# Performance work log

Hardware: AMD Instinct MI355X
Metric: run time of the kernel (lower is better)

The kernel has to match this reference:

```python
import jax, jax.numpy as jnp
import numpy as np

EMBED = 128
HEADS = 16
N = 10000
E = 160000
NEG_SLOPE = 0.2


def setup_inputs() -> dict:
    key = jax.random.key(0)
    ks = jax.random.split(key, 12)
    s = 0.05
    return {
        "x": jax.random.normal(ks[0], (N, EMBED), jnp.float32),
        "edge_index": jax.random.randint(ks[1], (2, E), 0, N, jnp.int64),
        # gat1: in=EMBED, out=EMBED, heads=16, concat
        "W1": jax.random.normal(ks[2], (EMBED, HEADS * EMBED), jnp.float32) * s,
        "a_src1": jax.random.normal(ks[3], (HEADS, EMBED), jnp.float32) * s,
        "a_dst1": jax.random.normal(ks[4], (HEADS, EMBED), jnp.float32) * s,
        "b1": jnp.zeros((HEADS * EMBED,), jnp.float32),
        # gat2: in=HEADS*EMBED, out=EMBED, heads=1, no concat
        "W2": jax.random.normal(ks[5], (HEADS * EMBED, EMBED), jnp.float32) * s,
        "a_src2": jax.random.normal(ks[6], (1, EMBED), jnp.float32) * s,
        "a_dst2": jax.random.normal(ks[7], (1, EMBED), jnp.float32) * s,
        "b2": jnp.zeros((EMBED,), jnp.float32),
        # classifier
        "Wc": jax.random.normal(ks[8], (EMBED, 1), jnp.float32) * s,
        "bc": jnp.zeros((1,), jnp.float32),
    }


def _gat_layer(x, src, dst, W, a_src, a_dst, b, heads, out_ch, n_nodes):
    # node projection: [N, H, C]
    h = (x @ W).reshape(n_nodes, heads, out_ch)
    # per-node attention logits [N, H]
    al_s = jnp.einsum('nhc,hc->nh', h, a_src)
    al_d = jnp.einsum('nhc,hc->nh', h, a_dst)
    # per-edge logits [E, H]
    e = jax.nn.leaky_relu(al_s[src] + al_d[dst], NEG_SLOPE)
    # segment softmax over incoming edges of each dst node
    m = jax.ops.segment_max(e, dst, num_segments=n_nodes)
    ex = jnp.exp(e - m[dst])
    z = jax.ops.segment_sum(ex, dst, num_segments=n_nodes)
    alpha = ex / (z[dst] + 1e-16)
    # weighted scatter-aggregate [N, H, C]
    msg = h[src] * alpha[:, :, None]
    out = jax.ops.segment_sum(msg, dst, num_segments=n_nodes)
    return out.reshape(n_nodes, heads * out_ch) + b


def reference(x, edge_index, W1, a_src1, a_dst1, b1, W2, a_src2, a_dst2, b2, Wc, bc):
    n_nodes = x.shape[0]
    # PyG GATConv default: add self loops
    loop = jnp.arange(n_nodes, dtype=edge_index.dtype)
    src = jnp.concatenate([edge_index[0], loop])
    dst = jnp.concatenate([edge_index[1], loop])
    h = _gat_layer(x, src, dst, W1, a_src1, a_dst1, b1, HEADS, EMBED, n_nodes)
    h = jax.nn.elu(h)
    h = _gat_layer(h, src, dst, W2, a_src2, a_dst2, b2, 1, EMBED, n_nodes)
    return h @ Wc + bc  # [N, 1]
```

## Files before the change

### kernel.cpp

```cpp
#include <hip/hip_runtime.h>
#include <hip/hip_bf16.h>

#define EMBED 128
#define HEADS 16
#define NEG 0.2f
#define MAXE 256

typedef __attribute__((ext_vector_type(8))) short short8;
typedef __attribute__((ext_vector_type(4))) float floatx4;

static __device__ __forceinline__ float leaky(float x) { return x > 0.f ? x : NEG * x; }

static __device__ __forceinline__ short f2bf_bits(float f) {
  __hip_bfloat16 h = __float2bfloat16(f);
  union { __hip_bfloat16 b; short s; } u;
  u.b = h;
  return u.s;
}


__global__ void k_hist(const int* __restrict__ ei, int E, int N, int* __restrict__ deg) {
  int i = blockIdx.x * blockDim.x + threadIdx.x;
  int Et = E + N;
  if (i >= Et) return;
  int d = (i < E) ? ei[E + i] : (i - E);
  atomicAdd(&deg[d], 1);
}

__global__ __launch_bounds__(256) void k_scan1(const int* __restrict__ deg,
                                               int* __restrict__ excl,
                                               int* __restrict__ bsum, int n) {
  __shared__ int s[256];
  int i = blockIdx.x * 256 + threadIdx.x;
  int v = (i < n) ? deg[i] : 0;
  s[threadIdx.x] = v;
  __syncthreads();
  for (int d = 1; d < 256; d <<= 1) {
    int add = ((int)threadIdx.x >= d) ? s[threadIdx.x - d] : 0;
    __syncthreads();
    s[threadIdx.x] += add;
    __syncthreads();
  }
  if (i < n) excl[i] = s[threadIdx.x] - v;
  if (threadIdx.x == 255) bsum[blockIdx.x] = s[255];
}

__global__ void k_scan2(int* __restrict__ bsum, int nb) {
  if (threadIdx.x == 0 && blockIdx.x == 0) {
    int acc = 0;
    for (int i = 0; i < nb; ++i) { int v = bsum[i]; bsum[i] = acc; acc += v; }
  }
}

__global__ __launch_bounds__(256) void k_scan3(const int* __restrict__ deg,
                                               const int* __restrict__ excl,
                                               const int* __restrict__ bsum,
                                               int* __restrict__ row_ptr,
                                               int* __restrict__ cursor, int n) {
  int i = blockIdx.x * 256 + threadIdx.x;
  if (i < n) {
    int r = excl[i] + bsum[blockIdx.x];
    row_ptr[i] = r;
    cursor[i] = r;
    if (i == n - 1) row_ptr[n] = r + deg[i];
  }
}

__global__ void k_scatter(const int* __restrict__ ei, int E, int N,
                          int* __restrict__ cursor, int* __restrict__ csr_src) {
  int i = blockIdx.x * blockDim.x + threadIdx.x;
  int Et = E + N;
  if (i >= Et) return;
  int s = (i < E) ? ei[i] : (i - E);
  int d = (i < E) ? ei[E + i] : (i - E);
  int pos = atomicAdd(&cursor[d], 1);
  csr_src[pos] = s;
}


__global__ __launch_bounds__(256) void k_prepAll(const float* __restrict__ W1,
                                                 const float* __restrict__ a_src1,
                                                 const float* __restrict__ a_dst1,
                                                 const float* __restrict__ W2,
                                                 const float* __restrict__ a_src2,
                                                 const float* __restrict__ a_dst2,
                                                 const float* __restrict__ Wc,
                                                 const float* __restrict__ b2,
                                                 const float* __restrict__ bc,
                                                 float* __restrict__ wsAll,
                                                 float* __restrict__ uvec,
                                                 float* __restrict__ cconst) {
  int gid = blockIdx.x * 256 + threadIdx.x;
  if (gid < 4096) {
    int sel = gid >> 11;
    int id = gid & 2047;
    int h = id >> 7, k = id & 127;
    const float* av = sel ? a_dst1 : a_src1;
    float sum = 0.f;
    const float* wrow = W1 + (size_t)k * 2048 + h * 128;
    const float* arow = av + h * 128;
#pragma unroll 4
    for (int c = 0; c < 128; ++c) sum += wrow[c] * arow[c];
    wsAll[gid] = sum;
  } else if (gid < 10240) {
    int g = gid - 4096;
    int sel = g >> 11;
    int k = g & 2047;
    const float* v = sel == 0 ? Wc : (sel == 1 ? a_src2 : a_dst2);
    const float* wrow = W2 + (size_t)k * 128;
    float s = 0.f;
#pragma unroll 4
    for (int j = 0; j < 128; ++j) s += wrow[j] * v[j];
    uvec[g] = s;
  } else if (gid == 10240) {
    float s = 0.f;
    for (int j = 0; j < 128; ++j) s += b2[j] * Wc[j];
    *cconst = s + bc[0];
  }
}


__global__ __launch_bounds__(256) void k_prep2aT(const float* __restrict__ W1,
                                                 short* __restrict__ hi,
                                                 short* __restrict__ lo) {
  __shared__ float tile[64][65];
  int h = blockIdx.x;
  int c0 = blockIdx.y * 64;
  int j0 = blockIdx.z * 64;
  int t = threadIdx.x;
#pragma unroll
  for (int i = 0; i < 4; ++i) {
    int idx4 = i * 256 + t;
    int c = idx4 >> 4, j4 = idx4 & 15;
    float4 v = *(const float4*)&W1[(size_t)(c0 + c) * 2048 + h * 128 + j0 + j4 * 4];
    tile[c][j4 * 4 + 0] = v.x;
    tile[c][j4 * 4 + 1] = v.y;
    tile[c][j4 * 4 + 2] = v.z;
    tile[c][j4 * 4 + 3] = v.w;
  }
  __syncthreads();
#pragma unroll
  for (int i = 0; i < 4; ++i) {
    int idx = i * 256 + t;
    int j = idx >> 4, c4 = idx & 15;
    unsigned short vh[4], vl[4];
#pragma unroll
    for (int ii = 0; ii < 4; ++ii) {
      float wv = tile[c4 * 4 + ii][j];
      short hb = f2bf_bits(wv);
      float hf = __uint_as_float(((unsigned int)(unsigned short)hb) << 16);
      vh[ii] = (unsigned short)hb;
      vl[ii] = (unsigned short)f2bf_bits(wv - hf);
    }
    size_t o = (size_t)h * 16384 + (size_t)(j0 + j) * 128 + c0 + c4 * 4;
    *(ushort4*)&hi[o] = make_ushort4(vh[0], vh[1], vh[2], vh[3]);
    *(ushort4*)&lo[o] = make_ushort4(vl[0], vl[1], vl[2], vl[3]);
  }
}


__global__ __launch_bounds__(256) void k_al1v2(const float* __restrict__ x,
                                               const float* __restrict__ wsAll,
                                               float* __restrict__ als,
                                               float* __restrict__ ald, int N) {
  __shared__ float wss[128][16], wsd[128][16];
  int tid = threadIdx.x;
  for (int i = tid; i < 2048; i += 256) {
    int h = i >> 7, c = i & 127;
    wss[c][h] = wsAll[i];
    wsd[c][h] = wsAll[2048 + i];
  }
  __syncthreads();
  int gid = blockIdx.x * 256 + tid;
  int n = gid >> 4, h = gid & 15;
  if (n >= N) return;
  const float4* xp = (const float4*)(x + (size_t)n * 128);
  float ps = 0.f, pd = 0.f;
#pragma unroll 8
  for (int c4 = 0; c4 < 32; ++c4) {
    float4 xv = xp[c4];
    int c = c4 * 4;
    ps += xv.x * wss[c][h] + xv.y * wss[c + 1][h] + xv.z * wss[c + 2][h] + xv.w * wss[c + 3][h];
    pd += xv.x * wsd[c][h] + xv.y * wsd[c + 1][h] + xv.z * wsd[c + 2][h] + xv.w * wsd[c + 3][h];
  }
  als[gid] = ps;
  ald[gid] = pd;
}


__global__ __launch_bounds__(256) void k_attn1d(const float* __restrict__ x,
                                                const float* __restrict__ als,
                                                const float* __restrict__ ald,
                                                const int* __restrict__ row_ptr,
                                                const int* __restrict__ csr,
                                                __hip_bfloat16* __restrict__ xaggb,
                                                int N) {
  int d = blockIdx.x;
  int tid = threadIdx.x;
  int e0 = row_ptr[d];
  int deg = row_ptr[d + 1] - e0;

  __shared__ int srcb[MAXE];
  __shared__ float ex[MAXE][17];
  __shared__ float xs[16][132];
  __shared__ float red[16][17];
  __shared__ float ald_sh[16], iz_sh[16];

  if (tid < 16) ald_sh[tid] = ald[(size_t)d * 16 + tid];
  __syncthreads();

  int hh = tid & 15, er = tid >> 4;
  float aldh = ald_sh[hh];
  int cg = tid & 15, h2 = tid >> 4;
  float acc[8] = {0.f, 0.f, 0.f, 0.f, 0.f, 0.f, 0.f, 0.f};

  if (deg <= MAXE) {
    for (int e = tid; e < deg; e += 256) srcb[e] = csr[e0 + e];
    __syncthreads();
    float zp = 0.f;
    for (int e = er; e < deg; e += 16) {
      float v = __expf(leaky(als[(size_t)srcb[e] * 16 + hh] + aldh));
      ex[e][hh] = v;
      zp += v;
    }
    red[er][hh] = zp;
    __syncthreads();
    if (tid < 16) {
      float z = 0.f;
#pragma unroll
      for (int k = 0; k < 16; ++k) z += red[k][tid];
      iz_sh[tid] = 1.f / (z + 1e-16f);
    }
    for (int base = 0; base < deg; base += 16) {
      int nb = min(16, deg - base);
      if (er < nb) {
        const float* xr = x + (size_t)srcb[base + er] * 128;
        *(float4*)&xs[er][cg * 4]      = *(const float4*)&xr[cg * 4];
        *(float4*)&xs[er][64 + cg * 4] = *(const float4*)&xr[64 + cg * 4];
      }
      __syncthreads();
      for (int e = 0; e < nb; ++e) {
        float a = ex[base + e][h2];
        float4 v0 = *(const float4*)&xs[e][cg * 4];
        float4 v1 = *(const float4*)&xs[e][64 + cg * 4];
        acc[0] += a * v0.x; acc[1] += a * v0.y; acc[2] += a * v0.z; acc[3] += a * v0.w;
        acc[4] += a * v1.x; acc[5] += a * v1.y; acc[6] += a * v1.z; acc[7] += a * v1.w;
      }
      __syncthreads();
    }
  } else {
    float zp = 0.f;
    for (int e = er; e < deg; e += 16) {
      int s = csr[e0 + e];
      zp += __expf(leaky(als[(size_t)s * 16 + hh] + aldh));
    }
    red[er][hh] = zp;
    __syncthreads();
    if (tid < 16) {
      float z = 0.f;
#pragma unroll
      for (int k = 0; k < 16; ++k) z += red[k][tid];
      iz_sh[tid] = 1.f / (z + 1e-16f);
    }
    for (int base = 0; base < deg; base += 16) {
      int nb = min(16, deg - base);
      __syncthreads();
      if (tid < nb) srcb[tid] = csr[e0 + base + tid];
      __syncthreads();
      if (tid < nb * 16) {
        int e = tid >> 4;
        ex[e][hh] = __expf(leaky(als[(size_t)srcb[e] * 16 + hh] + aldh));
      }
      if (er < nb) {
        const float* xr = x + (size_t)srcb[er] * 128;
        *(float4*)&xs[er][cg * 4]      = *(const float4*)&xr[cg * 4];
        *(float4*)&xs[er][64 + cg * 4] = *(const float4*)&xr[64 + cg * 4];
      }
      __syncthreads();
      for (int e = 0; e < nb; ++e) {
        float a = ex[e][h2];
        float4 v0 = *(const float4*)&xs[e][cg * 4];
        float4 v1 = *(const float4*)&xs[e][64 + cg * 4];
        acc[0] += a * v0.x; acc[1] += a * v0.y; acc[2] += a * v0.z; acc[3] += a * v0.w;
        acc[4] += a * v1.x; acc[5] += a * v1.y; acc[6] += a * v1.z; acc[7] += a * v1.w;
      }
    }
    __syncthreads();
  }

  float izh = iz_sh[h2];
  __hip_bfloat16 t0[4], t1[4];
#pragma unroll
  for (int i = 0; i < 4; ++i) {
    t0[i] = __float2bfloat16(acc[i] * izh);
    t1[i] = __float2bfloat16(acc[4 + i] * izh);
  }
  __hip_bfloat16* op = xaggb + (size_t)h2 * N * 128 + (size_t)d * 128;
  *(uint2*)&op[cg * 4]      = *(uint2*)t0;
  *(uint2*)&op[64 + cg * 4] = *(uint2*)t1;
}


__global__ __launch_bounds__(256, 2) void k_fused(const __hip_bfloat16* __restrict__ xaggb,
                                                  const short* __restrict__ w1t_hi,
                                                  const short* __restrict__ w1t_lo,
                                                  const float* __restrict__ b1,
                                                  const float* __restrict__ uvec,
                                                  float* __restrict__ partc,
                                                  float* __restrict__ parts,
                                                  float* __restrict__ partd,
                                                  int N) {
  __shared__ float sh[512];
  __shared__ __align__(16) char Bh[32768];
  __shared__ __align__(16) char Bl[32768];
  int tid = threadIdx.x;
  int h = blockIdx.y;
  int n0 = blockIdx.x * 256;

  for (int i = tid; i < 512; i += 256) {
    int arr = i >> 7, jj = i & 127;
    sh[i] = (arr == 0) ? b1[h * 128 + jj] : uvec[(arr - 1) * 2048 + h * 128 + jj];
  }
  const char* gbh = (const char*)(w1t_hi + (size_t)h * 16384);
  const char* gbl = (const char*)(w1t_lo + (size_t)h * 16384);
#pragma unroll
  for (int i = 0; i < 8; ++i) {
    int ci = i * 256 + tid;
    int row = ci >> 4, kc = ci & 15;
    int po = row * 256 + ((kc ^ (row & 15)) << 4);
    *(uint4*)(Bh + po) = *(const uint4*)(gbh + ci * 16);
    *(uint4*)(Bl + po) = *(const uint4*)(gbl + ci * 16);
  }

  int w = tid >> 6, lane = tid & 63;
  int quad = lane >> 4, l15 = lane & 15;
  int nw = n0 + w * 64;

  const char* abase = (const char*)xaggb + (size_t)h * N * 256;
  short8 a[4][4];
#pragma unroll
  for (int mt = 0; mt < 4; ++mt) {
    int node = nw + mt * 16 + l15;
    if (node >= N) node = N - 1;
    const char* rowp = abase + (size_t)node * 256 + quad * 16;
#pragma unroll
    for (int ks = 0; ks < 4; ++ks)
      a[mt][ks] = *(const short8*)(rowp + ks * 64);
  }
  __syncthreads();

  float ucr[8], usr[8], udr[8];
  floatx4 acc[4][8];
#pragma unroll
  for (int jt = 0; jt < 8; ++jt) {
    int jl = jt * 16 + l15;
    float b = sh[jl];
    ucr[jt] = sh[128 + jl];
    usr[jt] = sh[256 + jl];
    udr[jt] = sh[384 + jl];
#pragma unroll
    for (int mt = 0; mt < 4; ++mt) acc[mt][jt] = (floatx4)(b);
  }

  for (int ks = 0; ks < 4; ++ks) {
    int xo = (((ks * 4 + quad) ^ l15) << 4);
#pragma unroll
    for (int jt = 0; jt < 8; ++jt) {
      int po = (jt * 16 + l15) * 256 + xo;
      short8 wh = *(const short8*)(Bh + po);
      short8 wl = *(const short8*)(Bl + po);
#pragma unroll
      for (int mt = 0; mt < 4; ++mt) {
        acc[mt][jt] = __builtin_amdgcn_mfma_f32_16x16x32_bf16(a[mt][ks], wh, acc[mt][jt], 0, 0, 0);
        acc[mt][jt] = __builtin_amdgcn_mfma_f32_16x16x32_bf16(a[mt][ks], wl, acc[mt][jt], 0, 0, 0);
      }
    }
  }

#pragma unroll
  for (int mt = 0; mt < 4; ++mt) {
#pragma unroll
    for (int r = 0; r < 4; ++r) {
      int node = nw + mt * 16 + quad * 4 + r;
      float pc = 0.f, ps = 0.f, pd = 0.f;
#pragma unroll
      for (int jt = 0; jt < 8; ++jt) {
        float v = acc[mt][jt][r];
        float e = v > 0.f ? v : expm1f(v);
        pc += e * ucr[jt];
        ps += e * usr[jt];
        pd += e * udr[jt];
      }
#pragma unroll
      for (int off = 1; off <= 8; off <<= 1) {
        pc += __shfl_xor(pc, off);
        ps += __shfl_xor(ps, off);
        pd += __shfl_xor(pd, off);
      }
      if (l15 == 0 && node < N) {
        atomicAdd(&partc[node], pc);
        atomicAdd(&parts[node], ps);
        atomicAdd(&partd[node], pd);
      }
    }
  }
}


__global__ __launch_bounds__(256) void k_attn2s(const float* __restrict__ partc,
                                                const float* __restrict__ parts,
                                                const float* __restrict__ partd,
                                                const int* __restrict__ row_ptr,
                                                const int* __restrict__ csr,
                                                const float* __restrict__ cconst,
                                                float* __restrict__ out, int N) {
  int w = threadIdx.x >> 6, lane = threadIdx.x & 63;
  int d = blockIdx.x * 4 + w;
  if (d >= N) return;
  int e0 = row_ptr[d], deg = row_ptr[d + 1] - e0;
  float aldd = partd[d];
  float z = 0.f, num = 0.f;
  for (int e = lane; e < deg; e += 64) {
    int s = csr[e0 + e];
    float v = __expf(leaky(parts[s] + aldd));
    z += v;
    num += v * partc[s];
  }
#pragma unroll
  for (int off = 32; off; off >>= 1) {
    z += __shfl_xor(z, off);
    num += __shfl_xor(num, off);
  }
  if (lane == 0) out[d] = num / (z + 1e-16f) + cconst[0];
}


extern "C" void kernel_launch(void* const* d_in, const int* in_sizes, int n_in,
                              void* d_out, int out_size, void* d_ws, size_t ws_size,
                              hipStream_t stream) {
  const float* x      = (const float*)d_in[0];
  const int*   ei     = (const int*)d_in[1];
  const float* W1     = (const float*)d_in[2];
  const float* a_src1 = (const float*)d_in[3];
  const float* a_dst1 = (const float*)d_in[4];
  const float* b1     = (const float*)d_in[5];
  const float* W2     = (const float*)d_in[6];
  const float* a_src2 = (const float*)d_in[7];
  const float* a_dst2 = (const float*)d_in[8];
  const float* b2     = (const float*)d_in[9];
  const float* Wc     = (const float*)d_in[10];
  const float* bc     = (const float*)d_in[11];

  int N = in_sizes[0] / EMBED;
  int E = in_sizes[1] / 2;
  int Et = E + N;
  int nScanB = (N + 255) / 256;

  char* ws = (char*)d_ws;
  size_t off = 0;
  auto alloc = [&](size_t bytes) -> void* {
    void* p = ws + off;
    off += (bytes + 255) & ~(size_t)255;
    return p;
  };
  __hip_bfloat16* xaggb = (__hip_bfloat16*)alloc((size_t)N * 2048 * 2 + 65536);
  short* w1t_hi = (short*)alloc((size_t)262144 * 2);
  short* w1t_lo = (short*)alloc((size_t)262144 * 2);
  float* wsAll  = (float*)alloc(4096 * 4);
  float* uvec   = (float*)alloc(6144 * 4);
  float* cconst = (float*)alloc(256);
  float* als1   = (float*)alloc((size_t)N * 16 * 4);
  float* ald1   = (float*)alloc((size_t)N * 16 * 4);
  float* part   = (float*)alloc((size_t)3 * N * 4);
  float* partc  = part;
  float* parts  = part + N;
  float* partd  = part + 2 * N;
  int* deg      = (int*)alloc((size_t)N * 4);
  int* excl     = (int*)alloc((size_t)N * 4);
  int* bsum     = (int*)alloc((size_t)(nScanB + 1) * 4);
  int* row_ptr  = (int*)alloc((size_t)(N + 1) * 4);
  int* cursor   = (int*)alloc((size_t)N * 4);
  int* csr      = (int*)alloc((size_t)Et * 4);

  hipMemsetAsync(deg, 0, (size_t)N * 4, stream);
  hipMemsetAsync(part, 0, (size_t)3 * N * 4, stream);

  k_hist<<<(Et + 255) / 256, 256, 0, stream>>>(ei, E, N, deg);
  k_scan1<<<nScanB, 256, 0, stream>>>(deg, excl, bsum, N);
  k_scan2<<<1, 64, 0, stream>>>(bsum, nScanB);
  k_scan3<<<nScanB, 256, 0, stream>>>(deg, excl, bsum, row_ptr, cursor, N);
  k_scatter<<<(Et + 255) / 256, 256, 0, stream>>>(ei, E, N, cursor, csr);

  k_prepAll<<<41, 256, 0, stream>>>(W1, a_src1, a_dst1, W2, a_src2, a_dst2, Wc, b2, bc,
                                    wsAll, uvec, cconst);
  k_prep2aT<<<dim3(16, 2, 2), 256, 0, stream>>>(W1, w1t_hi, w1t_lo);

  k_al1v2<<<(N * 16 + 255) / 256, 256, 0, stream>>>(x, wsAll, als1, ald1, N);
  k_attn1d<<<N, 256, 0, stream>>>(x, als1, ald1, row_ptr, csr, xaggb, N);

  k_fused<<<dim3((N + 255) / 256, 16), 256, 0, stream>>>(xaggb, w1t_hi, w1t_lo, b1, uvec,
                                                         partc, parts, partd, N);
  k_attn2s<<<(N + 3) / 4, 256, 0, stream>>>(partc, parts, partd, row_ptr, csr, cconst,
                                            (float*)d_out, N);
}
```

Measured before the change: 216.3 us.

## Use one wavefront per node for layer-1 attention and transpose fused MFMA epilogue

The layer-1 attention aggregation moves from one 256-thread block per destination node, with shared-memory staging and many barriers, to one 64-lane wavefront per node. Each lane holds two channels for all 16 heads and gets attention weights by shuffles, with no LDS or __syncthreads. The fused GEMM kernel swaps its MFMA operands so each lane holds outputs for a single node. Its ELU/projection epilogue then reduces across quads with two shuffles instead of four per row, and replaces expm1f with __expf-1. The risks are serial per-edge gather latency inside each wave and slightly lower ELU accuracy near zero.

```diff
diff --git a/kernel.cpp b/kernel.cpp
--- a/kernel.cpp
+++ b/kernel.cpp
@@ -4,7 +4,6 @@
 #define EMBED 128
 #define HEADS 16
 #define NEG 0.2f
-#define MAXE 256
 
 typedef __attribute__((ext_vector_type(8))) short short8;
 typedef __attribute__((ext_vector_type(4))) float floatx4;
@@ -188,116 +187,59 @@
 }
 
 
-__global__ __launch_bounds__(256) void k_attn1d(const float* __restrict__ x,
+__global__ __launch_bounds__(256) void k_attn1w(const float* __restrict__ x,
                                                 const float* __restrict__ als,
                                                 const float* __restrict__ ald,
                                                 const int* __restrict__ row_ptr,
                                                 const int* __restrict__ csr,
                                                 __hip_bfloat16* __restrict__ xaggb,
                                                 int N) {
-  int d = blockIdx.x;
   int tid = threadIdx.x;
+  int d = blockIdx.x * 4 + (tid >> 6);
+  if (d >= N) return;
+  int lane = tid & 63;
+  int h = lane & 15, es = lane >> 4;
+  int grp = lane & 48;
+
   int e0 = row_ptr[d];
   int deg = row_ptr[d + 1] - e0;
 
-  __shared__ int srcb[MAXE];
-  __shared__ float ex[MAXE][17];
-  __shared__ float xs[16][132];
-  __shared__ float red[16][17];
-  __shared__ float ald_sh[16], iz_sh[16];
-
-  if (tid < 16) ald_sh[tid] = ald[(size_t)d * 16 + tid];
-  __syncthreads();
-
-  int hh = tid & 15, er = tid >> 4;
-  float aldh = ald_sh[hh];
-  int cg = tid & 15, h2 = tid >> 4;
-  float acc[8] = {0.f, 0.f, 0.f, 0.f, 0.f, 0.f, 0.f, 0.f};
-
-  if (deg <= MAXE) {
-    for (int e = tid; e < deg; e += 256) srcb[e] = csr[e0 + e];
-    __syncthreads();
-    float zp = 0.f;
-    for (int e = er; e < deg; e += 16) {
-      float v = __expf(leaky(als[(size_t)srcb[e] * 16 + hh] + aldh));
-      ex[e][hh] = v;
-      zp += v;
+  float aldh = ald[(size_t)d * 16 + h];
+
+  float zp = 0.f;
+  for (int e = es; e < deg; e += 4) {
+    int s = csr[e0 + e];
+    zp += __expf(leaky(als[(size_t)s * 16 + h] + aldh));
+  }
+  zp += __shfl_xor(zp, 16);
+  zp += __shfl_xor(zp, 32);
+  float iz = 1.f / (zp + 1e-16f);
+
+  float accx[16], accy[16];
+#pragma unroll
+  for (int k = 0; k < 16; ++k) { accx[k] = 0.f; accy[k] = 0.f; }
+
+  const float* xc = x + lane * 2;
+  for (int e = 0; e < deg; ++e) {
+    int s = csr[e0 + e];
+    float ev = __expf(leaky(als[(size_t)s * 16 + h] + aldh)) * iz;
+    float2 xv = *(const float2*)(xc + (size_t)s * 128);
+#pragma unroll
+    for (int k = 0; k < 16; ++k) {
+      float a = __shfl(ev, grp | k);
+      accx[k] += a * xv.x;
+      accy[k] += a * xv.y;
     }
-    red[er][hh] = zp;
-    __syncthreads();
-    if (tid < 16) {
-      float z = 0.f;
-#pragma unroll
-      for (int k = 0; k < 16; ++k) z += red[k][tid];
-      iz_sh[tid] = 1.f / (z + 1e-16f);
-    }
-    for (int base = 0; base < deg; base += 16) {
-      int nb = min(16, deg - base);
-      if (er < nb) {
-        const float* xr = x + (size_t)srcb[base + er] * 128;
-        *(float4*)&xs[er][cg * 4]      = *(const float4*)&xr[cg * 4];
-        *(float4*)&xs[er][64 + cg * 4] = *(const float4*)&xr[64 + cg * 4];
-      }
-      __syncthreads();
-      for (int e = 0; e < nb; ++e) {
-        float a = ex[base + e][h2];
-        float4 v0 = *(const float4*)&xs[e][cg * 4];
-        float4 v1 = *(const float4*)&xs[e][64 + cg * 4];
-        acc[0] += a * v0.x; acc[1] += a * v0.y; acc[2] += a * v0.z; acc[3] += a * v0.w;
-        acc[4] += a * v1.x; acc[5] += a * v1.y; acc[6] += a * v1.z; acc[7] += a * v1.w;
-      }
-      __syncthreads();
-    }
-  } else {
-    float zp = 0.f;
-    for (int e = er; e < deg; e += 16) {
-      int s = csr[e0 + e];
-      zp += __expf(leaky(als[(size_t)s * 16 + hh] + aldh));
-    }
-    red[er][hh] = zp;
-    __syncthreads();
-    if (tid < 16) {
-      float z = 0.f;
-#pragma unroll
-      for (int k = 0; k < 16; ++k) z += red[k][tid];
-      iz_sh[tid] = 1.f / (z + 1e-16f);
-    }
-    for (int base = 0; base < deg; base += 16) {
-      int nb = min(16, deg - base);
-      __syncthreads();
-      if (tid < nb) srcb[tid] = csr[e0 + base + tid];
-      __syncthreads();
-      if (tid < nb * 16) {
-        int e = tid >> 4;
-        ex[e][hh] = __expf(leaky(als[(size_t)srcb[e] * 16 + hh] + aldh));
-      }
-      if (er < nb) {
-        const float* xr = x + (size_t)srcb[er] * 128;
-        *(float4*)&xs[er][cg * 4]      = *(const float4*)&xr[cg * 4];
-        *(float4*)&xs[er][64 + cg * 4] = *(const float4*)&xr[64 + cg * 4];
-      }
-      __syncthreads();
-      for (int e = 0; e < nb; ++e) {
-        float a = ex[e][h2];
-        float4 v0 = *(const float4*)&xs[e][cg * 4];
-        float4 v1 = *(const float4*)&xs[e][64 + cg * 4];
-        acc[0] += a * v0.x; acc[1] += a * v0.y; acc[2] += a * v0.z; acc[3] += a * v0.w;
-        acc[4] += a * v1.x; acc[5] += a * v1.y; acc[6] += a * v1.z; acc[7] += a * v1.w;
-      }
-    }
-    __syncthreads();
-  }
-
-  float izh = iz_sh[h2];
-  __hip_bfloat16 t0[4], t1[4];
-#pragma unroll
-  for (int i = 0; i < 4; ++i) {
-    t0[i] = __float2bfloat16(acc[i] * izh);
-    t1[i] = __float2bfloat16(acc[4 + i] * izh);
-  }
-  __hip_bfloat16* op = xaggb + (size_t)h2 * N * 128 + (size_t)d * 128;
-  *(uint2*)&op[cg * 4]      = *(uint2*)t0;
-  *(uint2*)&op[64 + cg * 4] = *(uint2*)t1;
+  }
+
+  __hip_bfloat16* op = xaggb + (size_t)d * 128 + lane * 2;
+#pragma unroll
+  for (int k = 0; k < 16; ++k) {
+    __hip_bfloat16 t[2];
+    t[0] = __float2bfloat16(accx[k]);
+    t[1] = __float2bfloat16(accy[k]);
+    *(unsigned int*)(op + (size_t)k * N * 128) = *(unsigned int*)t;
+  }
 }
 
 
@@ -339,27 +281,22 @@
   const char* abase = (const char*)xaggb + (size_t)h * N * 256;
   short8 a[4][4];
 #pragma unroll
-  for (int mt = 0; mt < 4; ++mt) {
-    int node = nw + mt * 16 + l15;
+  for (int nt = 0; nt < 4; ++nt) {
+    int node = nw + nt * 16 + l15;
     if (node >= N) node = N - 1;
     const char* rowp = abase + (size_t)node * 256 + quad * 16;
 #pragma unroll
     for (int ks = 0; ks < 4; ++ks)
-      a[mt][ks] = *(const short8*)(rowp + ks * 64);
+      a[nt][ks] = *(const short8*)(rowp + ks * 64);
   }
   __syncthreads();
 
-  float ucr[8], usr[8], udr[8];
   floatx4 acc[4][8];
 #pragma unroll
   for (int jt = 0; jt < 8; ++jt) {
-    int jl = jt * 16 + l15;
-    float b = sh[jl];
-    ucr[jt] = sh[128 + jl];
-    usr[jt] = sh[256 + jl];
-    udr[jt] = sh[384 + jl];
-#pragma unroll
-    for (int mt = 0; mt < 4; ++mt) acc[mt][jt] = (floatx4)(b);
+    floatx4 bb = *(const floatx4*)&sh[jt * 16 + quad * 4];
+#pragma unroll
+    for (int nt = 0; nt < 4; ++nt) acc[nt][jt] = bb;
   }
 
   for (int ks = 0; ks < 4; ++ks) {
@@ -370,38 +307,44 @@
       short8 wh = *(const short8*)(Bh + po);
       short8 wl = *(const short8*)(Bl + po);
 #pragma unroll
-      for (int mt = 0; mt < 4; ++mt) {
-        acc[mt][jt] = __builtin_amdgcn_mfma_f32_16x16x32_bf16(a[mt][ks], wh, acc[mt][jt], 0, 0, 0);
-        acc[mt][jt] = __builtin_amdgcn_mfma_f32_16x16x32_bf16(a[mt][ks], wl, acc[mt][jt], 0, 0, 0);
+      for (int nt = 0; nt < 4; ++nt) {
+        acc[nt][jt] = __builtin_amdgcn_mfma_f32_16x16x32_bf16(wh, a[nt][ks], acc[nt][jt], 0, 0, 0);
+        acc[nt][jt] = __builtin_amdgcn_mfma_f32_16x16x32_bf16(wl, a[nt][ks], acc[nt][jt], 0, 0, 0);
       }
     }
   }
 
-#pragma unroll
-  for (int mt = 0; mt < 4; ++mt) {
-#pragma unroll
-    for (int r = 0; r < 4; ++r) {
-      int node = nw + mt * 16 + quad * 4 + r;
-      float pc = 0.f, ps = 0.f, pd = 0.f;
-#pragma unroll
-      for (int jt = 0; jt < 8; ++jt) {
-        float v = acc[mt][jt][r];
-        float e = v > 0.f ? v : expm1f(v);
-        pc += e * ucr[jt];
-        ps += e * usr[jt];
-        pd += e * udr[jt];
+  float pc[4] = {0.f, 0.f, 0.f, 0.f};
+  float ps[4] = {0.f, 0.f, 0.f, 0.f};
+  float pd[4] = {0.f, 0.f, 0.f, 0.f};
+#pragma unroll
+  for (int jt = 0; jt < 8; ++jt) {
+    floatx4 uc = *(const floatx4*)&sh[128 + jt * 16 + quad * 4];
+    floatx4 us = *(const floatx4*)&sh[256 + jt * 16 + quad * 4];
+    floatx4 ud = *(const floatx4*)&sh[384 + jt * 16 + quad * 4];
+#pragma unroll
+    for (int nt = 0; nt < 4; ++nt) {
+#pragma unroll
+      for (int r = 0; r < 4; ++r) {
+        float v = acc[nt][jt][r];
+        float e = v > 0.f ? v : (__expf(v) - 1.f);
+        pc[nt] += e * uc[r];
+        ps[nt] += e * us[r];
+        pd[nt] += e * ud[r];
       }
-#pragma unroll
-      for (int off = 1; off <= 8; off <<= 1) {
-        pc += __shfl_xor(pc, off);
-        ps += __shfl_xor(ps, off);
-        pd += __shfl_xor(pd, off);
-      }
-      if (l15 == 0 && node < N) {
-        atomicAdd(&partc[node], pc);
-        atomicAdd(&parts[node], ps);
-        atomicAdd(&partd[node], pd);
-      }
+    }
+  }
+#pragma unroll
+  for (int nt = 0; nt < 4; ++nt) {
+    float c = pc[nt], s = ps[nt], dd = pd[nt];
+    c += __shfl_xor(c, 16); c += __shfl_xor(c, 32);
+    s += __shfl_xor(s, 16); s += __shfl_xor(s, 32);
+    dd += __shfl_xor(dd, 16); dd += __shfl_xor(dd, 32);
+    int node = nw + nt * 16 + l15;
+    if (quad == 0 && node < N) {
+      atomicAdd(&partc[node], c);
+      atomicAdd(&parts[node], s);
+      atomicAdd(&partd[node], dd);
     }
   }
 }
@@ -496,7 +439,7 @@
   k_prep2aT<<<dim3(16, 2, 2), 256, 0, stream>>>(W1, w1t_hi, w1t_lo);
 
   k_al1v2<<<(N * 16 + 255) / 256, 256, 0, stream>>>(x, wsAll, als1, ald1, N);
-  k_attn1d<<<N, 256, 0, stream>>>(x, als1, ald1, row_ptr, csr, xaggb, N);
+  k_attn1w<<<(N + 3) / 4, 256, 0, stream>>>(x, als1, ald1, row_ptr, csr, xaggb, N);
 
   k_fused<<<dim3((N + 255) / 256, 16), 256, 0, stream>>>(xaggb, w1t_hi, w1t_lo, b1, uvec,
                                                          partc, parts, partd, N);
```

Result: faster. 203.7 us (-5.8%).
